# Kernel optimization log

Measured on AMD Instinct MI355X. Metric: run time of the kernel, lower is better.

The kernel has to match this reference:

```python
import jax, jax.numpy as jnp
import numpy as np

WIDTH = 64
RANK = 4
CLEVEL = 1
MLEVEL = 2
NB = 4
HID1, HID2 = 64, 128  # DenseNet hidden sizes for phi/psi kernel networks


def setup_inputs() -> dict:
    key = jax.random.key(0)
    ks = jax.random.split(key, 24)
    b, s = 2, 256

    def g(k, shape, fan):
        return jax.random.normal(k, shape, jnp.float32) / np.sqrt(fan)

    L = MLEVEL + 1
    inp = {
        "x": jax.random.normal(ks[0], (b, s, s, 1), jnp.float32),
        "a": jax.random.uniform(ks[1], (b, s, s, 2), jnp.float32),
        # lifting p: Linear(3, width)
        "pW": g(ks[2], (3, WIDTH), 3), "pb": jnp.zeros((WIDTH,), jnp.float32),
        # projection q: DenseNet([width, 2*width, 1], ReLU)
        "q1W": g(ks[3], (WIDTH, 2 * WIDTH), WIDTH), "q1b": jnp.zeros((2 * WIDTH,), jnp.float32),
        "q2W": g(ks[4], (2 * WIDTH, 1), 2 * WIDTH), "q2b": jnp.zeros((1,), jnp.float32),
        # low-rank kernel nets phi/psi: DenseNet([3, 64, 128, width*rank]), one per block (stacked)
        "phiW1": g(ks[5], (NB, 3, HID1), 3), "phib1": jnp.zeros((NB, HID1), jnp.float32),
        "phiW2": g(ks[6], (NB, HID1, HID2), HID1), "phib2": jnp.zeros((NB, HID2), jnp.float32),
        "phiW3": g(ks[7], (NB, HID2, WIDTH * RANK), HID2), "phib3": jnp.zeros((NB, WIDTH * RANK), jnp.float32),
        "psiW1": g(ks[8], (NB, 3, HID1), 3), "psib1": jnp.zeros((NB, HID1), jnp.float32),
        "psiW2": g(ks[9], (NB, HID1, HID2), HID1), "psib2": jnp.zeros((NB, HID2), jnp.float32),
        "psiW3": g(ks[10], (NB, HID2, WIDTH * RANK), HID2), "psib3": jnp.zeros((NB, WIDTH * RANK), jnp.float32),
        # per-block LayerNorm(width)
        "lnG": jnp.ones((NB, WIDTH), jnp.float32), "lnB": jnp.zeros((NB, WIDTH), jnp.float32),
        # per-block multi-level local-correction 3x3 convs (OIHW), levels 0..MLEVEL
        "convW": g(ks[11], (NB, L, WIDTH, WIDTH, 3, 3), WIDTH * 9),
        "convb": jnp.zeros((NB, L, WIDTH), jnp.float32),
    }
    return inp


def _mlp3(x, W1, b1, W2, b2, W3, b3):
    h = jax.nn.relu(x @ W1 + b1)
    h = jax.nn.relu(h @ W2 + b2)
    return h @ W3 + b3


def _lowrank(v, a, phi_p, psi_p):
    # v: (b, sx, sy, w) features; a: (b, sx, sy, 3) coords+input
    b, sx, sy, w = v.shape
    n = sx * sy
    af = a.reshape(b, n, 3)
    vf = v.reshape(b, n, w)
    phi = _mlp3(af, *phi_p).reshape(b, n, w, RANK)  # (b,n,w,r)
    psi = _mlp3(af, *psi_p).reshape(b, n, w, RANK)
    # K(u)(x_m) = sum_r phi_r(x_m) * (1/n) sum_n psi_r(y_n) u(y_n), per channel
    y = jnp.einsum("bnwr,bnw->bwr", psi, vf) / n
    out = jnp.einsum("bnwr,bwr->bnw", phi, y)
    return out.reshape(b, sx, sy, w)


def _conv3x3(x, W, bias):
    # x: (b,c,h,w) NCHW, W: (o,i,3,3)
    y = jax.lax.conv_general_dilated(x, W, (1, 1), "SAME",
                                     dimension_numbers=("NCHW", "OIHW", "NCHW"))
    return y + bias[None, :, None, None]


def _local_correction(xc, Ws, bs):
    # xc: (b,c,h,w); Ws: (L,o,i,3,3); multi-level conv pyramid, bilinear upsample back
    h, w = xc.shape[2], xc.shape[3]
    out = _conv3x3(xc, Ws[0], bs[0])
    for l in range(1, Ws.shape[0]):
        xl = xc[:, :, :: 2 ** l, :: 2 ** l]
        yl = _conv3x3(xl, Ws[l], bs[l])
        out = out + jax.image.resize(yl, yl.shape[:2] + (h, w), method="bilinear")
    return out


def _layernorm(x, g, b, eps=1e-5):
    mu = jnp.mean(x, axis=-1, keepdims=True)
    var = jnp.mean(jnp.square(x - mu), axis=-1, keepdims=True)
    return (x - mu) * jax.lax.rsqrt(var + eps) * g + b


def reference(x, a, pW, pb, q1W, q1b, q2W, q2b,
              phiW1, phib1, phiW2, phib2, phiW3, phib3,
              psiW1, psib1, psiW2, psib2, psiW3, psib3,
              lnG, lnB, convW, convb):
    b, sx, sy, _ = x.shape
    xa = jnp.concatenate([a, x], axis=-1)  # (b,sx,sy,3)
    acat = xa
    h = xa @ pW + pb  # lift to width
    c = 2 ** CLEVEL
    for i in range(NB):
        # local correction branch (NCHW conv pyramid)
        x1 = _local_correction(h.transpose(0, 3, 1, 2), convW[i], convb[i]).transpose(0, 2, 3, 1)
        # low-rank kernel integral on coarsened grid, then bilinear upsample
        hd = h[:, ::c, ::c]
        ad = acat[:, ::c, ::c]
        x2 = _lowrank(hd, ad,
                      (phiW1[i], phib1[i], phiW2[i], phib2[i], phiW3[i], phib3[i]),
                      (psiW1[i], psib1[i], psiW2[i], psib2[i], psiW3[i], psib3[i]))
        x2 = jax.image.resize(x2.transpose(0, 3, 1, 2), (b, WIDTH, sx, sy),
                              method="bilinear").transpose(0, 2, 3, 1)
        h = _layernorm(x1 + x2, lnG[i], lnB[i])
        if i != NB - 1:
            h = jax.nn.relu(h)
    h1 = jax.nn.relu(h @ q1W + q1b)
    return h1 @ q2W + q2b
```

## Files before the change

### kernel.cpp

```cpp
#include <hip/hip_runtime.h>
#include <cstddef>
#include <cstdint>


static constexpr size_t OFF_X1     = 0;
static constexpr size_t OFF_YL1    = 4194304;
static constexpr size_t OFF_YL2    = 5242880;
static constexpr size_t OFF_HBF    = 5505024;
static constexpr size_t OFF_H2PSI  = 9699328;
static constexpr size_t OFF_H2PHI  = 11796480;
static constexpr size_t OFF_CWTBF  = 13893632;
static constexpr size_t OFF_Q1BF   = 14114816;
static constexpr size_t OFF_W2T    = 14118912;
static constexpr size_t OFF_GPART  = 14151680;
static constexpr size_t OFF_SVP    = 18345984;
static constexpr size_t OFF_G      = 18378752;
static constexpr size_t OFF_SV     = 18395136;
static constexpr size_t OFF_C      = 18395264;
static constexpr size_t OFF_D      = 18411648;

typedef __attribute__((ext_vector_type(8)))  short bf16x8_t;
typedef __attribute__((ext_vector_type(16))) float f32x16_t;

__device__ inline float wave_sum64(float v) {
    v += __shfl_xor(v, 1);
    v += __shfl_xor(v, 2);
    v += __shfl_xor(v, 4);
    v += __shfl_xor(v, 8);
    v += __shfl_xor(v, 16);
    v += __shfl_xor(v, 32);
    return v;
}

__device__ inline unsigned short f2bf(float f) {
    uint32_t u = __float_as_uint(f);
    uint32_t r = u + 0x7FFFu + ((u >> 16) & 1u);
    return (unsigned short)(r >> 16);
}
__device__ inline float bf2f(unsigned short u) {
    return __uint_as_float((uint32_t)u << 16);
}
__device__ inline void bf8_to_f(uint4 u, float* d) {
    unsigned uv[4] = {u.x, u.y, u.z, u.w};
#pragma unroll
    for (int i = 0; i < 4; ++i) {
        d[2 * i]     = __uint_as_float((uv[i] & 0xFFFFu) << 16);
        d[2 * i + 1] = __uint_as_float(uv[i] & 0xFFFF0000u);
    }
}

__device__ inline size_t fullpix(int b, int n) {
    return (size_t)(b * 65536 + (n >> 7) * 512 + ((n & 127) << 1));
}

struct Lerp { int i0, i1; float f; };
__device__ inline Lerp lcoord(int o, float r, float off, int Sin) {
    float s = fmaxf(fmaf((float)o, r, off), 0.f);
    Lerp L;
    L.i0 = (int)s;
    L.f  = s - (float)L.i0;
    L.i1 = min(L.i0 + 1, Sin - 1);
    return L;
}

__global__ __launch_bounds__(256) void k_setup(const float* __restrict__ convW,
                                               unsigned short* __restrict__ cwt,
                                               const float* __restrict__ q1W,
                                               unsigned short* __restrict__ q1bf,
                                               const float* __restrict__ psiW2,
                                               const float* __restrict__ phiW2,
                                               unsigned short* __restrict__ w2t,
                                               const float* __restrict__ x,
                                               const float* __restrict__ a,
                                               const float* __restrict__ pW,
                                               const float* __restrict__ pb,
                                               unsigned short* __restrict__ hbf) {
    int bid = blockIdx.x;
    int t = threadIdx.x;
    if (bid < 1728) {
        int idx = bid * 256 + t;
        if (idx >= 442368) return;
        int j    = idx & 7;
        int oc   = (idx >> 3) & 63;
        int hi   = (idx >> 9) & 1;
        int kq   = (idx >> 10) & 3;
        int rest = idx >> 12;
        int tap  = rest % 9;
        int il   = rest / 9;
        int ic   = kq * 16 + hi * 8 + j;
        cwt[idx] = f2bf(convW[((size_t)(il * 64 + oc) * 64 + ic) * 9 + tap]);
    } else if (bid < 1760) {
        int idx = (bid - 1728) * 256 + t;
        int k = idx & 63;
        int j = idx >> 6;
        q1bf[j * 64 + k] = f2bf(q1W[k * 128 + j]);
    } else if (bid < 2016) {
        int idx = (bid - 1760) * 256 + t;
        int jj = idx & 7;
        int lo = (idx >> 3) & 31;
        int hi = (idx >> 8) & 1;
        int kq = (idx >> 9) & 3;
        int jt = (idx >> 11) & 3;
        int i  = (idx >> 13) & 3;
        int m  = idx >> 15;
        int k  = kq * 16 + hi * 8 + jj;
        int j  = jt * 32 + lo;
        const float* W2 = m ? phiW2 : psiW2;
        w2t[idx] = f2bf(W2[(size_t)i * 8192 + k * 128 + j]);
    } else {
        int p = (bid - 2016) * 256 + t;
        float a0 = a[(size_t)p * 2 + 0];
        float a1 = a[(size_t)p * 2 + 1];
        float xv = x[p];
        float vals[64];
#pragma unroll
        for (int c = 0; c < 64; ++c)
            vals[c] = fmaf(a0, pW[c], fmaf(a1, pW[64 + c], fmaf(xv, pW[128 + c], pb[c])));
        unsigned short us[64];
#pragma unroll
        for (int c = 0; c < 64; ++c) us[c] = f2bf(vals[c]);
        unsigned short* bp = hbf + (size_t)p * 64;
#pragma unroll
        for (int c = 0; c < 64; c += 8)
            *(uint4*)(bp + c) = *(uint4*)(us + c);
    }
}

__global__ __launch_bounds__(256) void k_convmlp(
    const unsigned short* __restrict__ hbf,
    const unsigned short* __restrict__ wbf,
    const float* __restrict__ convb,
    unsigned short* __restrict__ x1, unsigned short* __restrict__ yl1,
    unsigned short* __restrict__ yl2,
    const float* __restrict__ a, const float* __restrict__ x,
    const float* __restrict__ W1a, const float* __restrict__ b1a,
    const float* __restrict__ b2a,
    const float* __restrict__ W1b, const float* __restrict__ b1b,
    const float* __restrict__ b2b,
    const unsigned short* __restrict__ w2t,
    unsigned short* __restrict__ H2a, unsigned short* __restrict__ H2b,
    int iter) {
    __shared__ unsigned short Ald[11520];
    int bid = blockIdx.x;
    int t = threadIdx.x;

    if (bid >= 1344) {
        int blk = bid - 1344;
        int m = blk >> 9;
        int px0 = (blk & 511) << 6;
        const float* W1 = m ? W1b : W1a;
        const float* b1 = m ? b1b : b1a;
        const float* b2 = m ? b2b : b2a;
        unsigned short* H2 = m ? H2b : H2a;

        {
            int px = t >> 2;
            int ks = (t & 3) << 4;
            int pxl = px0 + px;
            int bb = pxl >> 14;
            size_t ap = fullpix(bb, pxl & 16383);
            float a0 = a[ap * 2], a1 = a[ap * 2 + 1], xv = x[ap];
            unsigned short hv[16];
#pragma unroll
            for (int q = 0; q < 16; ++q) {
                int k = ks + q;
                hv[q] = f2bf(fmaxf(fmaf(a0, W1[k], fmaf(a1, W1[64 + k],
                              fmaf(xv, W1[128 + k], b1[k]))), 0.f));
            }
            int base = px * 128 + ks * 2;
            int sw = (px & 7) << 4;
            *(uint4*)((char*)Ald + ((base) ^ sw))      = *(uint4*)hv;
            *(uint4*)((char*)Ald + ((base + 16) ^ sw)) = *(uint4*)(hv + 8);
        }
        __syncthreads();

        int w    = t >> 6;
        int lane = t & 63;
        int lo   = lane & 31;
        int hi   = lane >> 5;

        bf16x8_t faA[4], faB[4];
#pragma unroll
        for (int kq = 0; kq < 4; ++kq) {
            int koff = kq * 32 + hi * 16;
            int bytesA = (lo * 128 + koff) ^ ((lo & 7) << 4);
            int pxB = 32 + lo;
            int bytesB = (pxB * 128 + koff) ^ ((pxB & 7) << 4);
            faA[kq] = *(bf16x8_t*)((char*)Ald + bytesA);
            faB[kq] = *(bf16x8_t*)((char*)Ald + bytesB);
        }
        const unsigned short* wb =
            w2t + (size_t)(((m * 4 + iter) * 4 + w) * 4) * 512 + hi * 256 + lo * 8;
        f32x16_t accA = {}, accB = {};
#pragma unroll
        for (int kq = 0; kq < 4; ++kq) {
            bf16x8_t fb = *(const bf16x8_t*)(wb + kq * 512);
            accA = __builtin_amdgcn_mfma_f32_32x32x16_bf16(faA[kq], fb, accA, 0, 0, 0);
            accB = __builtin_amdgcn_mfma_f32_32x32x16_bf16(faB[kq], fb, accB, 0, 0, 0);
        }
        float bias2 = b2[w * 32 + lo];
#pragma unroll
        for (int reg = 0; reg < 16; ++reg) {
            int row = (reg & 3) + 8 * (reg >> 2) + 4 * hi;
            H2[(size_t)(px0 + row) * 128 + w * 32 + lo]      = f2bf(fmaxf(accA[reg] + bias2, 0.f));
            H2[(size_t)(px0 + 32 + row) * 128 + w * 32 + lo] = f2bf(fmaxf(accB[reg] + bias2, 0.f));
        }
        return;
    }

    int lvl, tix, Sl, st, tpb, tprx;
    if (bid < 1024)      { lvl = 0; tix = bid;        Sl = 256; st = 1; tpb = 512; tprx = 16; }
    else if (bid < 1280) { lvl = 1; tix = bid - 1024; Sl = 128; st = 2; tpb = 128; tprx = 8;  }
    else                 { lvl = 2; tix = bid - 1280; Sl = 64;  st = 4; tpb = 32;  tprx = 4;  }
    int b = tix / tpb;
    int r = tix - b * tpb;
    int y0 = (r / tprx) << 3, x0 = (r % tprx) << 4;

    for (int c = t; c < 1440; c += 256) {
        int lin = c >> 3, slot = c & 7;
        int ty = lin / 18, tx = lin - ty * 18;
        int oy = y0 + ty - 1, ox = x0 + tx - 1;
        uint4 val = make_uint4(0u, 0u, 0u, 0u);
        if ((unsigned)oy < (unsigned)Sl && (unsigned)ox < (unsigned)Sl) {
            const unsigned short* src =
                hbf + (((size_t)(b * 256 + oy * st) * 256 + ox * st) << 6) + (slot << 3);
            val = *(const uint4*)src;
        }
        int byte = (lin << 7) + (((slot ^ (lin & 7))) << 4);
        *(uint4*)((char*)Ald + byte) = val;
    }
    __syncthreads();

    int w    = t >> 6;
    int lane = t & 63;
    int lo   = lane & 31;
    int hi   = lane >> 5;
    f32x16_t acc00 = {}, acc01 = {};

    const unsigned short* wbase =
        wbf + (size_t)(iter * 3 + lvl) * 36864 + hi * 512 + lo * 8;

    int yA0 = 2 * w + (lo >> 4);
    int xA  = lo & 15;

    bf16x8_t v0c[4], v1c[4], v0n[4], v1n[4];
#pragma unroll
    for (int kq = 0; kq < 4; ++kq) {
        v0c[kq] = *(const bf16x8_t*)(wbase + kq * 1024);
        v1c[kq] = *(const bf16x8_t*)(wbase + kq * 1024 + 256);
    }
#pragma unroll
    for (int tap = 0; tap < 9; ++tap) {
        if (tap < 8) {
#pragma unroll
            for (int kq = 0; kq < 4; ++kq) {
                int keo = ((tap + 1) * 4 + kq) * 1024;
                v0n[kq] = *(const bf16x8_t*)(wbase + keo);
                v1n[kq] = *(const bf16x8_t*)(wbase + keo + 256);
            }
        }
        int dy = tap / 3, dx = tap - dy * 3;
        int lin0 = (yA0 + dy) * 18 + (xA + dx);
#pragma unroll
        for (int kq = 0; kq < 4; ++kq) {
            int icb = (kq << 5) + (hi << 4);
            int a0b = ((lin0 << 7) + icb) ^ ((lin0 & 7) << 4);
            bf16x8_t va0 = *(bf16x8_t*)((char*)Ald + a0b);
            acc00 = __builtin_amdgcn_mfma_f32_32x32x16_bf16(va0, v0c[kq], acc00, 0, 0, 0);
            acc01 = __builtin_amdgcn_mfma_f32_32x32x16_bf16(va0, v1c[kq], acc01, 0, 0, 0);
        }
#pragma unroll
        for (int kq = 0; kq < 4; ++kq) { v0c[kq] = v0n[kq]; v1c[kq] = v1n[kq]; }
    }

    unsigned short* out = (lvl == 0) ? x1 : (lvl == 1 ? yl1 : yl2);
    const float* bias = convb + (iter * 3 + lvl) * 64;
    float bias0 = bias[lo];
    float bias1 = bias[32 + lo];
#pragma unroll
    for (int reg = 0; reg < 16; ++reg) {
        int row = (reg & 3) + 8 * (reg >> 2) + 4 * hi;
        int yt  = 2 * w + (row >> 4);
        int xt  = row & 15;
        size_t pix = ((size_t)(b * Sl + y0 + yt) * Sl + (x0 + xt)) << 6;
        out[pix + lo]      = f2bf(acc00[reg] + bias0);
        out[pix + 32 + lo] = f2bf(acc01[reg] + bias1);
    }
}

__global__ __launch_bounds__(256) void k_gpart(const unsigned short* __restrict__ hbf,
                                               const unsigned short* __restrict__ H2psi,
                                               float* __restrict__ Gpart,
                                               float* __restrict__ svpart) {
    __shared__ unsigned short vtT[4096];
    __shared__ unsigned short h2tT[8192];
    int blk = blockIdx.x;
    int b = blk >> 8;
    int n0 = (blk & 255) << 6;
    int t = threadIdx.x;

    {
        int n = t >> 2, q = t & 3;
        const unsigned short* src = hbf + fullpix(b, n0 + n) * 64 + q * 16;
        unsigned short vv[16];
        *(uint4*)vv       = *(const uint4*)src;
        *(uint4*)(vv + 8) = *(const uint4*)(src + 8);
#pragma unroll
        for (int i = 0; i < 16; ++i) {
            int w = q * 16 + i;
            int byte = (w * 128 + n * 2) ^ ((w & 7) << 4);
            *(unsigned short*)((char*)vtT + byte) = vv[i];
        }
        const unsigned short* hsrc = H2psi + ((size_t)(b * 16384 + n0 + n)) * 128 + q * 32;
        unsigned short hh[32];
#pragma unroll
        for (int r = 0; r < 4; ++r)
            *(uint4*)(hh + r * 8) = *(const uint4*)(hsrc + r * 8);
#pragma unroll
        for (int i = 0; i < 32; ++i) {
            int k = q * 32 + i;
            int byte = (k * 128 + n * 2) ^ ((k & 7) << 4);
            *(unsigned short*)((char*)h2tT + byte) = hh[i];
        }
    }
    __syncthreads();

    int w    = t >> 6;
    int lane = t & 63;
    int lo   = lane & 31;
    int hi   = lane >> 5;
    int w0 = (w & 1) * 32;
    int c0 = (w >> 1) * 2;

    bf16x8_t fa[4];
#pragma unroll
    for (int kq = 0; kq < 4; ++kq) {
        int row = w0 + lo;
        int byte = (row * 128 + (kq * 16 + hi * 8) * 2) ^ ((row & 7) << 4);
        fa[kq] = *(bf16x8_t*)((char*)vtT + byte);
    }
    float* gp = Gpart + (size_t)blk * 8192;
#pragma unroll
    for (int ct = 0; ct < 2; ++ct) {
        int k0 = (c0 + ct) * 32;
        f32x16_t acc = {};
#pragma unroll
        for (int kq = 0; kq < 4; ++kq) {
            int krow = k0 + lo;
            int byte = (krow * 128 + (kq * 16 + hi * 8) * 2) ^ ((krow & 7) << 4);
            bf16x8_t fb = *(bf16x8_t*)((char*)h2tT + byte);
            acc = __builtin_amdgcn_mfma_f32_32x32x16_bf16(fa[kq], fb, acc, 0, 0, 0);
        }
#pragma unroll
        for (int reg = 0; reg < 16; ++reg) {
            int row = (reg & 3) + 8 * (reg >> 2) + 4 * hi;
            gp[(w0 + row) * 128 + k0 + lo] = acc[reg];
        }
    }

    if (t < 64) {
        float s = 0.f;
#pragma unroll
        for (int c = 0; c < 8; ++c) {
            int byte = (t * 128 + c * 16) ^ ((t & 7) << 4);
            uint4 u = *(uint4*)((char*)vtT + byte);
            float d[8];
            bf8_to_f(u, d);
            s += d[0]; s += d[1]; s += d[2]; s += d[3];
            s += d[4]; s += d[5]; s += d[6]; s += d[7];
        }
        svpart[blk * 64 + t] = s;
    }
}

__global__ __launch_bounds__(256) void k_gred(const float* __restrict__ Gpart,
                                              const float* __restrict__ svpart,
                                              float* __restrict__ G,
                                              float* __restrict__ sv) {
    __shared__ float red[4][64];
    int blk = blockIdx.x;
    int t = threadIdx.x;
    if (blk < 256) {
        int b  = blk >> 7;
        int es = (blk & 127) << 6;
        int e  = es + (t & 63);
        int cg = t >> 6;
        float s = 0.f;
        const float* gp = Gpart + ((size_t)(b * 256 + cg * 64)) * 8192 + e;
#pragma unroll 8
        for (int c = 0; c < 64; ++c) s += gp[(size_t)c * 8192];
        red[cg][t & 63] = s;
        __syncthreads();
        if (t < 64)
            G[b * 8192 + es + t] = red[0][t] + red[1][t] + red[2][t] + red[3][t];
    } else {
        int b = blk - 256;
        int w = t & 63, cg = t >> 6;
        float s = 0.f;
        const float* sp = svpart + ((size_t)(b * 256 + cg * 64)) * 64 + w;
#pragma unroll 8
        for (int c = 0; c < 64; ++c) s += sp[c * 64];
        red[cg][w] = s;
        __syncthreads();
        if (t < 64) sv[b * 64 + t] = red[0][t] + red[1][t] + red[2][t] + red[3][t];
    }
}

__global__ __launch_bounds__(256) void k_yc(const float* __restrict__ G,
                                            const float* __restrict__ sv,
                                            const float* __restrict__ W3psi,
                                            const float* __restrict__ b3psi,
                                            const float* __restrict__ W3phi,
                                            const float* __restrict__ b3phi,
                                            float* __restrict__ C,
                                            float* __restrict__ D) {
    __shared__ float ybar[256];
    int bq = blockIdx.x;
    int b = bq >> 4, q = bq & 15;
    int t = threadIdx.x;
    {
        int o = t, w = o >> 2;
        const float* gp = &G[(size_t)(b * 64 + w) * 128];
        float s0 = 0.f, s1 = 0.f, s2 = 0.f, s3 = 0.f;
#pragma unroll 4
        for (int k = 0; k < 128; k += 4) {
            s0 = fmaf(W3psi[(k + 0) * 256 + o], gp[k + 0], s0);
            s1 = fmaf(W3psi[(k + 1) * 256 + o], gp[k + 1], s1);
            s2 = fmaf(W3psi[(k + 2) * 256 + o], gp[k + 2], s2);
            s3 = fmaf(W3psi[(k + 3) * 256 + o], gp[k + 3], s3);
        }
        float s = b3psi[o] * sv[b * 64 + w] + ((s0 + s1) + (s2 + s3));
        ybar[o] = s * (1.f / 16384.f);
    }
    __syncthreads();
#pragma unroll
    for (int rep = 0; rep < 2; ++rep) {
        int e = q * 512 + rep * 256 + t;
        int w = e >> 7, k = e & 127;
        const float* wp = &W3phi[k * 256 + w * 4];
        C[b * 8192 + e] = fmaf(wp[0], ybar[w * 4],
                          fmaf(wp[1], ybar[w * 4 + 1],
                          fmaf(wp[2], ybar[w * 4 + 2], wp[3] * ybar[w * 4 + 3])));
    }
    if (q == 0 && t < 64) {
        int w = t;
        D[b * 64 + w] = b3phi[w * 4] * ybar[w * 4] + b3phi[w * 4 + 1] * ybar[w * 4 + 1]
                      + b3phi[w * 4 + 2] * ybar[w * 4 + 2] + b3phi[w * 4 + 3] * ybar[w * 4 + 3];
    }
}

__global__ __launch_bounds__(256) void k_x2c(const unsigned short* __restrict__ H2phi,
                                             const float* __restrict__ C,
                                             const float* __restrict__ D,
                                             unsigned short* __restrict__ x2c) {
    __shared__ float cl[8192];
    __shared__ float h2l[4096];
    __shared__ float Dl[64];
    int blk = blockIdx.x;
    int b = blk >> 9;
    int px0 = (blk & 511) << 5;
    int t = threadIdx.x;

    const float* cp = C + b * 8192;
#pragma unroll
    for (int r = 0; r < 8; ++r) {
        int f = r * 1024 + t * 4;
        *(float4*)&cl[f] = *(const float4*)&cp[f];
    }
    if (t < 64) Dl[t] = D[b * 64 + t];
    {
        const unsigned short* hsrc = H2phi + ((size_t)(b * 16384 + px0)) * 128;
#pragma unroll
        for (int r = 0; r < 2; ++r) {
            int f = r * 2048 + t * 8;
            uint4 u = *(const uint4*)(hsrc + f);
            float d[8];
            bf8_to_f(u, d);
            int px = f >> 7;
            int sw2 = ((px & 7) << 4) ^ (((px >> 3) & 1) << 6);
            *(float4*)((char*)h2l + ((f * 4) ^ sw2))      = make_float4(d[0], d[1], d[2], d[3]);
            *(float4*)((char*)h2l + ((f * 4 + 16) ^ sw2)) = make_float4(d[4], d[5], d[6], d[7]);
        }
    }
    __syncthreads();

    int px = t & 31;
    int w0 = (t >> 5) << 3;
    int psw = ((px & 7) << 4) ^ (((px >> 3) & 1) << 6);
    float acc[8];
#pragma unroll
    for (int j = 0; j < 8; ++j) acc[j] = 0.f;

#pragma unroll 4
    for (int kq = 0; kq < 32; ++kq) {
        float4 hq = *(float4*)((char*)h2l + ((px * 512 + kq * 16) ^ psw));
#pragma unroll
        for (int j = 0; j < 8; ++j) {
            float4 cq = *(float4*)&cl[(w0 + j) * 128 + kq * 4];
            acc[j] = fmaf(hq.x, cq.x, acc[j]);
            acc[j] = fmaf(hq.y, cq.y, acc[j]);
            acc[j] = fmaf(hq.z, cq.z, acc[j]);
            acc[j] = fmaf(hq.w, cq.w, acc[j]);
        }
    }
    unsigned short us[8];
#pragma unroll
    for (int j = 0; j < 8; ++j) us[j] = f2bf(acc[j] + Dl[w0 + j]);
    unsigned short* op = x2c + ((size_t)(b * 16384 + px0 + px)) * 64 + w0;
    *(uint4*)op = *(uint4*)us;
}

__global__ __launch_bounds__(256) void k_epilogue(const unsigned short* __restrict__ x1,
                                                  const unsigned short* __restrict__ yl1,
                                                  const unsigned short* __restrict__ yl2,
                                                  const unsigned short* __restrict__ x2c,
                                                  const float* __restrict__ lnG,
                                                  const float* __restrict__ lnB,
                                                  unsigned short* __restrict__ hbf,
                                                  int do_relu) {
    __shared__ float y1s[2][10][64];
    __shared__ float xcs[2][10][64];
    __shared__ float y2s[2][6][64];
    int t    = threadIdx.x;
    int blk  = blockIdx.x;
    int b    = blk >> 12;
    int rest = blk & 4095;
    int y    = rest >> 4;
    int x0   = (rest & 15) << 4;
    int wv = t >> 6, lane = t & 63;

    Lerp ly1 = lcoord(y, 0.5f, -0.25f, 128);
    Lerp ly2 = lcoord(y, 0.25f, -0.375f, 64);
    int c1 = max(0, (int)floorf((float)x0 * 0.5f - 0.25f));
    int c2 = max(0, (int)floorf((float)x0 * 0.25f - 0.375f));

    const unsigned short* Y1 = yl1 + (size_t)b * 16384 * 64;
    const unsigned short* Y2 = yl2 + (size_t)b * 4096 * 64;
    const unsigned short* XC = x2c + (size_t)b * 16384 * 64;
    for (int f4 = t; f4 < 832; f4 += 256) {
        int e, row, col;
        const unsigned short* src;
        float* dst;
        if (f4 < 320) {
            e = f4 * 4;
            int r = e / 640, rm = e - r * 640;
            int j = rm >> 6, ch = rm & 63;
            row = r ? ly1.i1 : ly1.i0;
            col = min(c1 + j, 127);
            src = &Y1[((size_t)(row * 128 + col)) * 64 + ch];
            dst = &y1s[r][j][ch];
        } else if (f4 < 640) {
            e = (f4 - 320) * 4;
            int r = e / 640, rm = e - r * 640;
            int j = rm >> 6, ch = rm & 63;
            row = r ? ly1.i1 : ly1.i0;
            col = min(c1 + j, 127);
            src = &XC[((size_t)(row * 128 + col)) * 64 + ch];
            dst = &xcs[r][j][ch];
        } else {
            e = (f4 - 640) * 4;
            int r = e / 384, rm = e - r * 384;
            int j = rm >> 6, ch = rm & 63;
            row = r ? ly2.i1 : ly2.i0;
            col = min(c2 + j, 63);
            src = &Y2[((size_t)(row * 64 + col)) * 64 + ch];
            dst = &y2s[r][j][ch];
        }
        uint2 u = *(const uint2*)src;
        dst[0] = __uint_as_float((u.x & 0xFFFFu) << 16);
        dst[1] = __uint_as_float(u.x & 0xFFFF0000u);
        dst[2] = __uint_as_float((u.y & 0xFFFFu) << 16);
        dst[3] = __uint_as_float(u.y & 0xFFFF0000u);
    }
    __syncthreads();

    float g = lnG[lane], be = lnB[lane];
    for (int pp = 0; pp < 4; ++pp) {
        int xx = x0 + wv * 4 + pp;
        size_t pix = (size_t)((b * 256 + y) * 256 + xx);
        float v = bf2f(x1[pix * 64 + lane]);
        {
            Lerp lx = lcoord(xx, 0.5f, -0.25f, 128);
            int j0 = lx.i0 - c1, j1 = lx.i1 - c1;
            float a0 = y1s[0][j0][lane], a1 = y1s[0][j1][lane];
            float b0 = y1s[1][j0][lane], b1 = y1s[1][j1][lane];
            float ta = a0 + lx.f * (a1 - a0);
            float tb = b0 + lx.f * (b1 - b0);
            v += ta + ly1.f * (tb - ta);
            float p0 = xcs[0][j0][lane], p1 = xcs[0][j1][lane];
            float q0 = xcs[1][j0][lane], q1 = xcs[1][j1][lane];
            float tp = p0 + lx.f * (p1 - p0);
            float tq = q0 + lx.f * (q1 - q0);
            v += tp + ly1.f * (tq - tp);
        }
        {
            Lerp lx = lcoord(xx, 0.25f, -0.375f, 64);
            int j0 = lx.i0 - c2, j1 = lx.i1 - c2;
            float a0 = y2s[0][j0][lane], a1 = y2s[0][j1][lane];
            float b0 = y2s[1][j0][lane], b1 = y2s[1][j1][lane];
            float ta = a0 + lx.f * (a1 - a0);
            float tb = b0 + lx.f * (b1 - b0);
            v += ta + ly2.f * (tb - ta);
        }
        float mu  = wave_sum64(v) * (1.f / 64.f);
        float d   = v - mu;
        float var = wave_sum64(d * d) * (1.f / 64.f);
        float ov  = fmaf(d * rsqrtf(var + 1e-5f), g, be);
        if (do_relu) ov = fmaxf(ov, 0.f);
        hbf[pix * 64 + lane] = f2bf(ov);
    }
}

__global__ __launch_bounds__(256) void k_head_mfma(
    const unsigned short* __restrict__ hbf,
    const unsigned short* __restrict__ q1bf,
    const float* __restrict__ q1b,
    const float* __restrict__ q2,
    const float* __restrict__ q2b,
    float* __restrict__ out) {
    __shared__ unsigned short Q[8192];
    int t = threadIdx.x;
    for (int c = t; c < 1024; c += 256) {
        int j = c >> 3, slot = c & 7;
        uint4 v = *(const uint4*)(q1bf + j * 64 + slot * 8);
        int byte = (j * 128 + slot * 16) ^ ((j & 7) << 4);
        *(uint4*)((char*)Q + byte) = v;
    }
    __syncthreads();

    int w = t >> 6, lane = t & 63;
    int lo = lane & 31, hi = lane >> 5;
    int px0 = blockIdx.x * 128 + w * 32;

    bf16x8_t av[4];
    const unsigned short* hp = hbf + (size_t)(px0 + lo) * 64 + hi * 8;
#pragma unroll
    for (int ks = 0; ks < 4; ++ks)
        av[ks] = *(const bf16x8_t*)(hp + ks * 16);

    float res[16];
#pragma unroll
    for (int r = 0; r < 16; ++r) res[r] = 0.f;

#pragma unroll
    for (int jb = 0; jb < 4; ++jb) {
        f32x16_t acc = {};
        int j = jb * 32 + lo;
#pragma unroll
        for (int ks = 0; ks < 4; ++ks) {
            int byte = (j * 128 + ks * 32 + hi * 16) ^ ((j & 7) << 4);
            bf16x8_t bv = *(bf16x8_t*)((char*)Q + byte);
            acc = __builtin_amdgcn_mfma_f32_32x32x16_bf16(av[ks], bv, acc, 0, 0, 0);
        }
        float b1 = q1b[j];
        float w2 = q2[j];
#pragma unroll
        for (int r = 0; r < 16; ++r)
            res[r] = fmaf(fmaxf(acc[r] + b1, 0.f), w2, res[r]);
    }
#pragma unroll
    for (int r = 0; r < 16; ++r) {
        float v = res[r];
        v += __shfl_xor(v, 1);
        v += __shfl_xor(v, 2);
        v += __shfl_xor(v, 4);
        v += __shfl_xor(v, 8);
        v += __shfl_xor(v, 16);
        res[r] = v;
    }
    if (lo == 0) {
        float qb = q2b[0];
#pragma unroll
        for (int r = 0; r < 16; ++r) {
            int row = (r & 3) + 8 * (r >> 2) + 4 * hi;
            out[px0 + row] = res[r] + qb;
        }
    }
}

extern "C" void kernel_launch(void* const* d_in, const int* in_sizes, int n_in,
                              void* d_out, int out_size, void* d_ws, size_t ws_size,
                              hipStream_t stream) {
    const float* x     = (const float*)d_in[0];
    const float* a     = (const float*)d_in[1];
    const float* pW    = (const float*)d_in[2];
    const float* pb    = (const float*)d_in[3];
    const float* q1W   = (const float*)d_in[4];
    const float* q1b   = (const float*)d_in[5];
    const float* q2W   = (const float*)d_in[6];
    const float* q2b   = (const float*)d_in[7];
    const float* phiW1 = (const float*)d_in[8];
    const float* phib1 = (const float*)d_in[9];
    const float* phiW2 = (const float*)d_in[10];
    const float* phib2 = (const float*)d_in[11];
    const float* phiW3 = (const float*)d_in[12];
    const float* phib3 = (const float*)d_in[13];
    const float* psiW1 = (const float*)d_in[14];
    const float* psib1 = (const float*)d_in[15];
    const float* psiW2 = (const float*)d_in[16];
    const float* psib2 = (const float*)d_in[17];
    const float* psiW3 = (const float*)d_in[18];
    const float* psib3 = (const float*)d_in[19];
    const float* lnG   = (const float*)d_in[20];
    const float* lnB   = (const float*)d_in[21];
    const float* convW = (const float*)d_in[22];
    const float* convb = (const float*)d_in[23];

    float* ws = (float*)d_ws;
    unsigned short* x1    = (unsigned short*)(ws + OFF_X1);
    unsigned short* yl1   = (unsigned short*)(ws + OFF_YL1);
    unsigned short* yl2   = (unsigned short*)(ws + OFF_YL2);
    unsigned short* hbf   = (unsigned short*)(ws + OFF_HBF);
    unsigned short* H2psi = (unsigned short*)(ws + OFF_H2PSI);
    unsigned short* x2c   = (unsigned short*)(ws + OFF_H2PSI);
    unsigned short* H2phi = (unsigned short*)(ws + OFF_H2PHI);
    unsigned short* cwtbf = (unsigned short*)(ws + OFF_CWTBF);
    unsigned short* q1bf  = (unsigned short*)(ws + OFF_Q1BF);
    unsigned short* w2t   = (unsigned short*)(ws + OFF_W2T);
    float* Gpart = ws + OFF_GPART;
    float* svpart= ws + OFF_SVP;
    float* G     = ws + OFF_G;
    float* sv    = ws + OFF_SV;
    float* C     = ws + OFF_C;
    float* D     = ws + OFF_D;

    k_setup<<<2528, 256, 0, stream>>>(convW, cwtbf, q1W, q1bf,
                                      psiW2, phiW2, w2t, x, a, pW, pb, hbf);

    for (int i = 0; i < 4; ++i) {
        k_convmlp<<<2368, 256, 0, stream>>>(hbf, cwtbf, convb, x1, yl1, yl2,
                                            a, x,
                                            psiW1 + i * 192, psib1 + i * 64, psib2 + i * 128,
                                            phiW1 + i * 192, phib1 + i * 64, phib2 + i * 128,
                                            w2t, H2psi, H2phi, i);
        k_gpart<<<512, 256, 0, stream>>>(hbf, H2psi, Gpart, svpart);
        k_gred<<<258, 256, 0, stream>>>(Gpart, svpart, G, sv);
        k_yc<<<32, 256, 0, stream>>>(G, sv,
                                     psiW3 + (size_t)i * 32768, psib3 + i * 256,
                                     phiW3 + (size_t)i * 32768, phib3 + i * 256,
                                     C, D);
        k_x2c<<<1024, 256, 0, stream>>>(H2phi, C, D, x2c);
        k_epilogue<<<8192, 256, 0, stream>>>(x1, yl1, yl2, x2c,
                                             lnG + i * 64, lnB + i * 64,
                                             hbf, (i < 3) ? 1 : 0);
    }

    k_head_mfma<<<1024, 256, 0, stream>>>(hbf, q1bf, q1b, q2W, q2b, (float*)d_out);
}
```

Measured before the change: 385.5 us.

## Fuse low-rank kernel stages into one cooperative kernel with grid syncs

Merges the Gram partial, reduction, coefficient and x2c-projection kernels into a single cooperative launch, with grid.sync() between the phases. The aim is to remove three kernel launches and their inter-kernel gaps per block iteration. The x2c phase now covers 64 pixels per block in two halves, so it runs on 512 blocks instead of 1024. C and D are addressed through sv offsets, and a no-op self-assignment is left in the code. The changes add grid-barrier cost and require all 512 blocks to be co-resident.

```diff
diff --git a/kernel.cpp b/kernel.cpp
--- a/kernel.cpp
+++ b/kernel.cpp
@@ -1,6 +1,9 @@
 #include <hip/hip_runtime.h>
+#include <hip/hip_cooperative_groups.h>
 #include <cstddef>
 #include <cstdint>
+
+namespace cg = cooperative_groups;
 
 
 static constexpr size_t OFF_X1     = 0;
@@ -288,226 +291,230 @@
     }
 }
 
-__global__ __launch_bounds__(256) void k_gpart(const unsigned short* __restrict__ hbf,
-                                               const unsigned short* __restrict__ H2psi,
-                                               float* __restrict__ Gpart,
-                                               float* __restrict__ svpart) {
-    __shared__ unsigned short vtT[4096];
-    __shared__ unsigned short h2tT[8192];
-    int blk = blockIdx.x;
-    int b = blk >> 8;
-    int n0 = (blk & 255) << 6;
-    int t = threadIdx.x;
-
-    {
-        int n = t >> 2, q = t & 3;
-        const unsigned short* src = hbf + fullpix(b, n0 + n) * 64 + q * 16;
-        unsigned short vv[16];
-        *(uint4*)vv       = *(const uint4*)src;
-        *(uint4*)(vv + 8) = *(const uint4*)(src + 8);
-#pragma unroll
-        for (int i = 0; i < 16; ++i) {
-            int w = q * 16 + i;
-            int byte = (w * 128 + n * 2) ^ ((w & 7) << 4);
-            *(unsigned short*)((char*)vtT + byte) = vv[i];
-        }
-        const unsigned short* hsrc = H2psi + ((size_t)(b * 16384 + n0 + n)) * 128 + q * 32;
-        unsigned short hh[32];
-#pragma unroll
-        for (int r = 0; r < 4; ++r)
-            *(uint4*)(hh + r * 8) = *(const uint4*)(hsrc + r * 8);
-#pragma unroll
-        for (int i = 0; i < 32; ++i) {
-            int k = q * 32 + i;
-            int byte = (k * 128 + n * 2) ^ ((k & 7) << 4);
-            *(unsigned short*)((char*)h2tT + byte) = hh[i];
-        }
-    }
-    __syncthreads();
-
-    int w    = t >> 6;
-    int lane = t & 63;
-    int lo   = lane & 31;
-    int hi   = lane >> 5;
-    int w0 = (w & 1) * 32;
-    int c0 = (w >> 1) * 2;
-
-    bf16x8_t fa[4];
-#pragma unroll
-    for (int kq = 0; kq < 4; ++kq) {
-        int row = w0 + lo;
-        int byte = (row * 128 + (kq * 16 + hi * 8) * 2) ^ ((row & 7) << 4);
-        fa[kq] = *(bf16x8_t*)((char*)vtT + byte);
-    }
-    float* gp = Gpart + (size_t)blk * 8192;
-#pragma unroll
-    for (int ct = 0; ct < 2; ++ct) {
-        int k0 = (c0 + ct) * 32;
-        f32x16_t acc = {};
-#pragma unroll
-        for (int kq = 0; kq < 4; ++kq) {
-            int krow = k0 + lo;
-            int byte = (krow * 128 + (kq * 16 + hi * 8) * 2) ^ ((krow & 7) << 4);
-            bf16x8_t fb = *(bf16x8_t*)((char*)h2tT + byte);
-            acc = __builtin_amdgcn_mfma_f32_32x32x16_bf16(fa[kq], fb, acc, 0, 0, 0);
-        }
-#pragma unroll
-        for (int reg = 0; reg < 16; ++reg) {
-            int row = (reg & 3) + 8 * (reg >> 2) + 4 * hi;
-            gp[(w0 + row) * 128 + k0 + lo] = acc[reg];
-        }
-    }
-
-    if (t < 64) {
-        float s = 0.f;
-#pragma unroll
-        for (int c = 0; c < 8; ++c) {
-            int byte = (t * 128 + c * 16) ^ ((t & 7) << 4);
-            uint4 u = *(uint4*)((char*)vtT + byte);
-            float d[8];
-            bf8_to_f(u, d);
-            s += d[0]; s += d[1]; s += d[2]; s += d[3];
-            s += d[4]; s += d[5]; s += d[6]; s += d[7];
-        }
-        svpart[blk * 64 + t] = s;
-    }
-}
-
-__global__ __launch_bounds__(256) void k_gred(const float* __restrict__ Gpart,
-                                              const float* __restrict__ svpart,
-                                              float* __restrict__ G,
-                                              float* __restrict__ sv) {
-    __shared__ float red[4][64];
+__global__ __launch_bounds__(256) void k_lowrank(
+    const unsigned short* __restrict__ hbf,
+    const unsigned short* __restrict__ H2psi,
+    float* __restrict__ Gpart, float* __restrict__ svpart,
+    float* __restrict__ G, float* __restrict__ sv,
+    const float* __restrict__ W3psi, const float* __restrict__ b3psi,
+    const float* __restrict__ W3phi, const float* __restrict__ b3phi,
+    const unsigned short* __restrict__ H2phi,
+    unsigned short* __restrict__ x2c) {
+    cg::grid_group grid = cg::this_grid();
+    __shared__ float smem[12352];
     int blk = blockIdx.x;
     int t = threadIdx.x;
-    if (blk < 256) {
-        int b  = blk >> 7;
-        int es = (blk & 127) << 6;
-        int e  = es + (t & 63);
-        int cg = t >> 6;
-        float s = 0.f;
-        const float* gp = Gpart + ((size_t)(b * 256 + cg * 64)) * 8192 + e;
+
+    {
+        unsigned short* vtT  = (unsigned short*)smem;
+        unsigned short* h2tT = vtT + 4096;
+        int b = blk >> 8;
+        int n0 = (blk & 255) << 6;
+        {
+            int n = t >> 2, q = t & 3;
+            const unsigned short* src = hbf + fullpix(b, n0 + n) * 64 + q * 16;
+            unsigned short vv[16];
+            *(uint4*)vv       = *(const uint4*)src;
+            *(uint4*)(vv + 8) = *(const uint4*)(src + 8);
+#pragma unroll
+            for (int i = 0; i < 16; ++i) {
+                int w = q * 16 + i;
+                int byte = (w * 128 + n * 2) ^ ((w & 7) << 4);
+                *(unsigned short*)((char*)vtT + byte) = vv[i];
+            }
+            const unsigned short* hsrc = H2psi + ((size_t)(b * 16384 + n0 + n)) * 128 + q * 32;
+            unsigned short hh[32];
+#pragma unroll
+            for (int r = 0; r < 4; ++r)
+                *(uint4*)(hh + r * 8) = *(const uint4*)(hsrc + r * 8);
+#pragma unroll
+            for (int i = 0; i < 32; ++i) {
+                int k = q * 32 + i;
+                int byte = (k * 128 + n * 2) ^ ((k & 7) << 4);
+                *(unsigned short*)((char*)h2tT + byte) = hh[i];
+            }
+        }
+        __syncthreads();
+
+        int w    = t >> 6;
+        int lane = t & 63;
+        int lo   = lane & 31;
+        int hi   = lane >> 5;
+        int w0 = (w & 1) * 32;
+        int c0 = (w >> 1) * 2;
+
+        bf16x8_t fa[4];
+#pragma unroll
+        for (int kq = 0; kq < 4; ++kq) {
+            int row = w0 + lo;
+            int byte = (row * 128 + (kq * 16 + hi * 8) * 2) ^ ((row & 7) << 4);
+            fa[kq] = *(bf16x8_t*)((char*)vtT + byte);
+        }
+        float* gp = Gpart + (size_t)blk * 8192;
+#pragma unroll
+        for (int ct = 0; ct < 2; ++ct) {
+            int k0 = (c0 + ct) * 32;
+            f32x16_t acc = {};
+#pragma unroll
+            for (int kq = 0; kq < 4; ++kq) {
+                int krow = k0 + lo;
+                int byte = (krow * 128 + (kq * 16 + hi * 8) * 2) ^ ((krow & 7) << 4);
+                bf16x8_t fb = *(bf16x8_t*)((char*)h2tT + byte);
+                acc = __builtin_amdgcn_mfma_f32_32x32x16_bf16(fa[kq], fb, acc, 0, 0, 0);
+            }
+#pragma unroll
+            for (int reg = 0; reg < 16; ++reg) {
+                int row = (reg & 3) + 8 * (reg >> 2) + 4 * hi;
+                gp[(w0 + row) * 128 + k0 + lo] = acc[reg];
+            }
+        }
+
+        if (t < 64) {
+            float s = 0.f;
+#pragma unroll
+            for (int c = 0; c < 8; ++c) {
+                int byte = (t * 128 + c * 16) ^ ((t & 7) << 4);
+                uint4 u = *(uint4*)((char*)vtT + byte);
+                float d[8];
+                bf8_to_f(u, d);
+                s += d[0]; s += d[1]; s += d[2]; s += d[3];
+                s += d[4]; s += d[5]; s += d[6]; s += d[7];
+            }
+            svpart[blk * 64 + t] = s;
+        }
+    }
+    grid.sync();
+
+    {
+        float (*red)[64] = (float(*)[64])smem;
+        if (blk < 256) {
+            int b  = blk >> 7;
+            int es = (blk & 127) << 6;
+            int e  = es + (t & 63);
+            int cg_ = t >> 6;
+            float s = 0.f;
+            const float* gp = Gpart + ((size_t)(b * 256 + cg_ * 64)) * 8192 + e;
 #pragma unroll 8
-        for (int c = 0; c < 64; ++c) s += gp[(size_t)c * 8192];
-        red[cg][t & 63] = s;
+            for (int c = 0; c < 64; ++c) s += gp[(size_t)c * 8192];
+            red[cg_][t & 63] = s;
+            __syncthreads();
+            if (t < 64)
+                G[b * 8192 + es + t] = red[0][t] + red[1][t] + red[2][t] + red[3][t];
+        } else if (blk < 258) {
+            int b = blk - 256;
+            int w = t & 63, cg_ = t >> 6;
+            float s = 0.f;
+            const float* sp = svpart + ((size_t)(b * 256 + cg_ * 64)) * 64 + w;
+#pragma unroll 8
+            for (int c = 0; c < 64; ++c) s += sp[c * 64];
+            red[cg_][w] = s;
+            __syncthreads();
+            if (t < 64) sv[b * 64 + t] = red[0][t] + red[1][t] + red[2][t] + red[3][t];
+        }
+    }
+    grid.sync();
+
+    {
+        float* ybar = smem;
+        if (blk < 32) {
+            int b = blk >> 4, q = blk & 15;
+            {
+                int o = t, w = o >> 2;
+                const float* gp = &G[(size_t)(b * 64 + w) * 128];
+                float s0 = 0.f, s1 = 0.f, s2 = 0.f, s3 = 0.f;
+#pragma unroll 4
+                for (int k = 0; k < 128; k += 4) {
+                    s0 = fmaf(W3psi[(k + 0) * 256 + o], gp[k + 0], s0);
+                    s1 = fmaf(W3psi[(k + 1) * 256 + o], gp[k + 1], s1);
+                    s2 = fmaf(W3psi[(k + 2) * 256 + o], gp[k + 2], s2);
+                    s3 = fmaf(W3psi[(k + 3) * 256 + o], gp[k + 3], s3);
+                }
+                float s = b3psi[o] * sv[b * 64 + w] + ((s0 + s1) + (s2 + s3));
+                ybar[o] = s * (1.f / 16384.f);
+            }
+            __syncthreads();
+#pragma unroll
+            for (int rep = 0; rep < 2; ++rep) {
+                int e = q * 512 + rep * 256 + t;
+                int w = e >> 7, k = e & 127;
+                const float* wp = &W3phi[k * 256 + w * 4];
+                (G + 16384)[0] = (G + 16384)[0];
+                ((float*)(sv + 128))[b * 8192 + e] = fmaf(wp[0], ybar[w * 4],
+                                  fmaf(wp[1], ybar[w * 4 + 1],
+                                  fmaf(wp[2], ybar[w * 4 + 2], wp[3] * ybar[w * 4 + 3])));
+            }
+            if (q == 0 && t < 64) {
+                int w = t;
+                ((float*)(sv + 128))[16384 + b * 64 + w] =
+                      b3phi[w * 4] * ybar[w * 4] + b3phi[w * 4 + 1] * ybar[w * 4 + 1]
+                    + b3phi[w * 4 + 2] * ybar[w * 4 + 2] + b3phi[w * 4 + 3] * ybar[w * 4 + 3];
+            }
+        }
+    }
+    grid.sync();
+
+    {
+        const float* C = (const float*)(sv + 128);
+        const float* D = C + 16384;
+        float* cl  = smem;
+        float* h2l = smem + 8192;
+        float* Dl  = smem + 8192 + 4096;
+        int b = blk >> 8;
+        int px0base = (blk & 255) << 6;
+
         __syncthreads();
-        if (t < 64)
-            G[b * 8192 + es + t] = red[0][t] + red[1][t] + red[2][t] + red[3][t];
-    } else {
-        int b = blk - 256;
-        int w = t & 63, cg = t >> 6;
-        float s = 0.f;
-        const float* sp = svpart + ((size_t)(b * 256 + cg * 64)) * 64 + w;
-#pragma unroll 8
-        for (int c = 0; c < 64; ++c) s += sp[c * 64];
-        red[cg][w] = s;
-        __syncthreads();
-        if (t < 64) sv[b * 64 + t] = red[0][t] + red[1][t] + red[2][t] + red[3][t];
-    }
-}
-
-__global__ __launch_bounds__(256) void k_yc(const float* __restrict__ G,
-                                            const float* __restrict__ sv,
-                                            const float* __restrict__ W3psi,
-                                            const float* __restrict__ b3psi,
-                                            const float* __restrict__ W3phi,
-                                            const float* __restrict__ b3phi,
-                                            float* __restrict__ C,
-                                            float* __restrict__ D) {
-    __shared__ float ybar[256];
-    int bq = blockIdx.x;
-    int b = bq >> 4, q = bq & 15;
-    int t = threadIdx.x;
-    {
-        int o = t, w = o >> 2;
-        const float* gp = &G[(size_t)(b * 64 + w) * 128];
-        float s0 = 0.f, s1 = 0.f, s2 = 0.f, s3 = 0.f;
+        const float* cp = C + b * 8192;
+#pragma unroll
+        for (int r = 0; r < 8; ++r) {
+            int f = r * 1024 + t * 4;
+            *(float4*)&cl[f] = *(const float4*)&cp[f];
+        }
+        if (t < 64) Dl[t] = D[b * 64 + t];
+
+        for (int half = 0; half < 2; ++half) {
+            int px0 = px0base + half * 32;
+            __syncthreads();
+            {
+                const unsigned short* hsrc = H2phi + ((size_t)(b * 16384 + px0)) * 128;
+#pragma unroll
+                for (int r = 0; r < 2; ++r) {
+                    int f = r * 2048 + t * 8;
+                    uint4 u = *(const uint4*)(hsrc + f);
+                    float d[8];
+                    bf8_to_f(u, d);
+                    int px = f >> 7;
+                    int sw2 = ((px & 7) << 4) ^ (((px >> 3) & 1) << 6);
+                    *(float4*)((char*)h2l + ((f * 4) ^ sw2))      = make_float4(d[0], d[1], d[2], d[3]);
+                    *(float4*)((char*)h2l + ((f * 4 + 16) ^ sw2)) = make_float4(d[4], d[5], d[6], d[7]);
+                }
+            }
+            __syncthreads();
+
+            int px = t & 31;
+            int w0 = (t >> 5) << 3;
+            int psw = ((px & 7) << 4) ^ (((px >> 3) & 1) << 6);
+            float acc[8];
+#pragma unroll
+            for (int j = 0; j < 8; ++j) acc[j] = 0.f;
 #pragma unroll 4
-        for (int k = 0; k < 128; k += 4) {
-            s0 = fmaf(W3psi[(k + 0) * 256 + o], gp[k + 0], s0);
-            s1 = fmaf(W3psi[(k + 1) * 256 + o], gp[k + 1], s1);
-            s2 = fmaf(W3psi[(k + 2) * 256 + o], gp[k + 2], s2);
-            s3 = fmaf(W3psi[(k + 3) * 256 + o], gp[k + 3], s3);
-        }
-        float s = b3psi[o] * sv[b * 64 + w] + ((s0 + s1) + (s2 + s3));
-        ybar[o] = s * (1.f / 16384.f);
-    }
-    __syncthreads();
-#pragma unroll
-    for (int rep = 0; rep < 2; ++rep) {
-        int e = q * 512 + rep * 256 + t;
-        int w = e >> 7, k = e & 127;
-        const float* wp = &W3phi[k * 256 + w * 4];
-        C[b * 8192 + e] = fmaf(wp[0], ybar[w * 4],
-                          fmaf(wp[1], ybar[w * 4 + 1],
-                          fmaf(wp[2], ybar[w * 4 + 2], wp[3] * ybar[w * 4 + 3])));
-    }
-    if (q == 0 && t < 64) {
-        int w = t;
-        D[b * 64 + w] = b3phi[w * 4] * ybar[w * 4] + b3phi[w * 4 + 1] * ybar[w * 4 + 1]
-                      + b3phi[w * 4 + 2] * ybar[w * 4 + 2] + b3phi[w * 4 + 3] * ybar[w * 4 + 3];
-    }
-}
-
-__global__ __launch_bounds__(256) void k_x2c(const unsigned short* __restrict__ H2phi,
-                                             const float* __restrict__ C,
-                                             const float* __restrict__ D,
-                                             unsigned short* __restrict__ x2c) {
-    __shared__ float cl[8192];
-    __shared__ float h2l[4096];
-    __shared__ float Dl[64];
-    int blk = blockIdx.x;
-    int b = blk >> 9;
-    int px0 = (blk & 511) << 5;
-    int t = threadIdx.x;
-
-    const float* cp = C + b * 8192;
-#pragma unroll
-    for (int r = 0; r < 8; ++r) {
-        int f = r * 1024 + t * 4;
-        *(float4*)&cl[f] = *(const float4*)&cp[f];
-    }
-    if (t < 64) Dl[t] = D[b * 64 + t];
-    {
-        const unsigned short* hsrc = H2phi + ((size_t)(b * 16384 + px0)) * 128;
-#pragma unroll
-        for (int r = 0; r < 2; ++r) {
-            int f = r * 2048 + t * 8;
-            uint4 u = *(const uint4*)(hsrc + f);
-            float d[8];
-            bf8_to_f(u, d);
-            int px = f >> 7;
-            int sw2 = ((px & 7) << 4) ^ (((px >> 3) & 1) << 6);
-            *(float4*)((char*)h2l + ((f * 4) ^ sw2))      = make_float4(d[0], d[1], d[2], d[3]);
-            *(float4*)((char*)h2l + ((f * 4 + 16) ^ sw2)) = make_float4(d[4], d[5], d[6], d[7]);
-        }
-    }
-    __syncthreads();
-
-    int px = t & 31;
-    int w0 = (t >> 5) << 3;
-    int psw = ((px & 7) << 4) ^ (((px >> 3) & 1) << 6);
-    float acc[8];
-#pragma unroll
-    for (int j = 0; j < 8; ++j) acc[j] = 0.f;
-
-#pragma unroll 4
-    for (int kq = 0; kq < 32; ++kq) {
-        float4 hq = *(float4*)((char*)h2l + ((px * 512 + kq * 16) ^ psw));
-#pragma unroll
-        for (int j = 0; j < 8; ++j) {
-            float4 cq = *(float4*)&cl[(w0 + j) * 128 + kq * 4];
-            acc[j] = fmaf(hq.x, cq.x, acc[j]);
-            acc[j] = fmaf(hq.y, cq.y, acc[j]);
-            acc[j] = fmaf(hq.z, cq.z, acc[j]);
-            acc[j] = fmaf(hq.w, cq.w, acc[j]);
-        }
-    }
-    unsigned short us[8];
-#pragma unroll
-    for (int j = 0; j < 8; ++j) us[j] = f2bf(acc[j] + Dl[w0 + j]);
-    unsigned short* op = x2c + ((size_t)(b * 16384 + px0 + px)) * 64 + w0;
-    *(uint4*)op = *(uint4*)us;
+            for (int kq = 0; kq < 32; ++kq) {
+                float4 hq = *(float4*)((char*)h2l + ((px * 512 + kq * 16) ^ psw));
+#pragma unroll
+                for (int j = 0; j < 8; ++j) {
+                    float4 cq = *(float4*)&cl[(w0 + j) * 128 + kq * 4];
+                    acc[j] = fmaf(hq.x, cq.x, acc[j]);
+                    acc[j] = fmaf(hq.y, cq.y, acc[j]);
+                    acc[j] = fmaf(hq.z, cq.z, acc[j]);
+                    acc[j] = fmaf(hq.w, cq.w, acc[j]);
+                }
+            }
+            unsigned short us[8];
+#pragma unroll
+            for (int j = 0; j < 8; ++j) us[j] = f2bf(acc[j] + Dl[w0 + j]);
+            unsigned short* op = x2c + ((size_t)(b * 16384 + px0 + px)) * 64 + w0;
+            *(uint4*)op = *(uint4*)us;
+        }
+    }
 }
 
 __global__ __launch_bounds__(256) void k_epilogue(const unsigned short* __restrict__ x1,
@@ -721,8 +728,6 @@
     float* svpart= ws + OFF_SVP;
     float* G     = ws + OFF_G;
     float* sv    = ws + OFF_SV;
-    float* C     = ws + OFF_C;
-    float* D     = ws + OFF_D;
 
     k_setup<<<2528, 256, 0, stream>>>(convW, cwtbf, q1W, q1bf,
                                       psiW2, phiW2, w2t, x, a, pW, pb, hbf);
@@ -733,13 +738,18 @@
                                             psiW1 + i * 192, psib1 + i * 64, psib2 + i * 128,
                                             phiW1 + i * 192, phib1 + i * 64, phib2 + i * 128,
                                             w2t, H2psi, H2phi, i);
-        k_gpart<<<512, 256, 0, stream>>>(hbf, H2psi, Gpart, svpart);
-        k_gred<<<258, 256, 0, stream>>>(Gpart, svpart, G, sv);
-        k_yc<<<32, 256, 0, stream>>>(G, sv,
-                                     psiW3 + (size_t)i * 32768, psib3 + i * 256,
-                                     phiW3 + (size_t)i * 32768, phib3 + i * 256,
-                                     C, D);
-        k_x2c<<<1024, 256, 0, stream>>>(H2phi, C, D, x2c);
+        const unsigned short* hbf_c   = hbf;
+        const unsigned short* H2psi_c = H2psi;
+        const unsigned short* H2phi_c = H2phi;
+        const float* W3psi_i = psiW3 + (size_t)i * 32768;
+        const float* b3psi_i = psib3 + i * 256;
+        const float* W3phi_i = phiW3 + (size_t)i * 32768;
+        const float* b3phi_i = phib3 + i * 256;
+        void* args[] = {(void*)&hbf_c, (void*)&H2psi_c, (void*)&Gpart, (void*)&svpart,
+                        (void*)&G, (void*)&sv,
+                        (void*)&W3psi_i, (void*)&b3psi_i, (void*)&W3phi_i, (void*)&b3phi_i,
+                        (void*)&H2phi_c, (void*)&x2c};
+        hipLaunchCooperativeKernel((void*)k_lowrank, dim3(512), dim3(256), args, 0, stream);
         k_epilogue<<<8192, 256, 0, stream>>>(x1, yl1, yl2, x2c,
                                              lnG + i * 64, lnB + i * 64,
                                              hbf, (i < 3) ? 1 : 0);
```

New measurement: 1.020 ms. +164.5%, slower.
